# Kernel tuning notes

Hardware: AMD Instinct MI355X
Metric: run time of the kernel (lower is better)

The kernel has to match this reference:

```python
import jax, jax.numpy as jnp
import numpy as np
import math

B, S, D, H = 2, 2048, 512, 8
DH = D // H  # 64

def setup_inputs() -> dict:
    key = jax.random.key(0)
    ks = jax.random.split(key, 7)
    x = jax.random.normal(ks[0], (B, S, D), jnp.float32)
    shift = jax.random.normal(ks[1], (B, S, S), jnp.float32)
    mask = jax.random.randint(ks[2], (B, S, S), 0, 2).astype(jnp.float32)
    W = jax.random.normal(ks[3], (3 * D, D), jnp.float32) / math.sqrt(D)
    b = jnp.zeros((3 * D,), jnp.float32)
    Wo = jax.random.normal(ks[4], (D, D), jnp.float32) / math.sqrt(D)
    bo = jnp.zeros((D,), jnp.float32)
    return {"x": x, "shift": shift, "mask": mask, "W": W, "b": b, "Wo": Wo, "bo": bo}

def reference(x, shift, mask, W, b, Wo, bo):
    # qkv projection: (B,S,3D). torch chunk(n_heads) then chunk(3) =>
    # per-head layout is [q_h | k_h | v_h] within each 3*DH-sized slice.
    qkv = x @ W.T + b
    qkv = qkv.reshape(B, S, H, 3, DH)
    qkv = jnp.moveaxis(qkv, (2, 3), (0, 1))  # (H, 3, B, S, DH)
    q, k, v = qkv[:, 0], qkv[:, 1], qkv[:, 2]  # each (H, B, S, DH)

    head_scale = jnp.exp2(-jnp.arange(H, dtype=jnp.float32)).reshape(H, 1, 1, 1)  # 2^-h
    logits = jnp.einsum('hbqd,hbkd->hbqk', q, k) / math.sqrt(DH)
    logits = logits - head_scale * shift[None]          # ALiBi-style per-head shift
    m = mask[None]                                       # (1,B,S,S)
    logits = logits * m - 1e8 * (1.0 - m)
    att = jax.nn.softmax(logits, axis=-1)
    o = jnp.einsum('hbqk,hbkd->hbqd', att, v)            # (H,B,S,DH)
    o = jnp.moveaxis(o, 0, 2).reshape(B, S, D)           # concat heads on last dim
    return o @ Wo.T + bo
```

## Files before the change

kernel.cpp:

```cpp
#include <hip/hip_runtime.h>
#include <math.h>

constexpr int Bc = 2, Sc = 2048, Dc = 512, Hc = 8, DHc = 64;
constexpr int NQKV = 3 * Dc;

typedef unsigned short u16;
typedef unsigned int u32;
typedef __attribute__((ext_vector_type(8))) __bf16 bf16x8;
typedef __attribute__((ext_vector_type(16))) float f32x16;

#define MFMA32 __builtin_amdgcn_mfma_f32_32x32x16_bf16

__device__ inline uint2 splitpack2(float a, float b) {
  u32 ua = __float_as_uint(a), ub = __float_as_uint(b);
  u32 hi = (ub & 0xFFFF0000u) | (ua >> 16);
  float ra = a - __uint_as_float(ua & 0xFFFF0000u);
  float rb = b - __uint_as_float(ub & 0xFFFF0000u);
  u32 lo = (__float_as_uint(rb) & 0xFFFF0000u) | (__float_as_uint(ra) >> 16);
  return uint2{hi, lo};
}
__device__ inline void split1(float v, u16& hi, u16& lo) {
  u32 u = __float_as_uint(v);
  hi = (u16)(u >> 16);
  float r = v - __uint_as_float(u & 0xFFFF0000u);
  lo = (u16)(__float_as_uint(r) >> 16);
}

__global__ __launch_bounds__(256, 2) void gemm1_mfma(
    const float* __restrict__ x, const float* __restrict__ W,
    const float* __restrict__ bias, u16* __restrict__ Qhi,
    u16* __restrict__ Qlo, u16* __restrict__ Khi, u16* __restrict__ Klo,
    u16* __restrict__ Vthi, u16* __restrict__ Vtlo) {
  __shared__ __align__(16) u16 pool[18432];
  const int tid = threadIdx.x;
  const int wave = tid >> 6, lane = tid & 63, l31 = lane & 31, lhi = lane >> 5;
  const int wm = wave >> 1, wn = wave & 1;
  const int m0 = blockIdx.y * 128, n0 = blockIdx.x * 64;

  f32x16 acc[2];
#pragma unroll
  for (int r = 0; r < 16; ++r) {
    acc[0][r] = 0.f;
    acc[1][r] = 0.f;
  }

  for (int k0 = 0; k0 < 512; k0 += 32) {
#pragma unroll
    for (int i = 0; i < 2; ++i) {
      const int g = i * 256 + tid;
      const int m = g >> 2, kg = g & 3;
      const float* src = x + (size_t)(m0 + m) * 512 + k0 + kg * 8;
      const float4 v0 = *(const float4*)src;
      const float4 v1 = *(const float4*)(src + 4);
      const uint2 p0 = splitpack2(v0.x, v0.y), p1 = splitpack2(v0.z, v0.w);
      const uint2 p2 = splitpack2(v1.x, v1.y), p3 = splitpack2(v1.z, v1.w);
      const int row = (kg & 1) * 32 + (m & 31);
      *(uint4*)&pool[((((0 * 4 + (m >> 5)) * 2 + (kg >> 1)) * 64 + row)) * 8] =
          uint4{p0.x, p1.x, p2.x, p3.x};
      *(uint4*)&pool[((((1 * 4 + (m >> 5)) * 2 + (kg >> 1)) * 64 + row)) * 8] =
          uint4{p0.y, p1.y, p2.y, p3.y};
    }
    {
      const int n = tid >> 2, kg = tid & 3;
      const float* src = W + (size_t)(n0 + n) * 512 + k0 + kg * 8;
      const float4 v0 = *(const float4*)src;
      const float4 v1 = *(const float4*)(src + 4);
      const uint2 p0 = splitpack2(v0.x, v0.y), p1 = splitpack2(v0.z, v0.w);
      const uint2 p2 = splitpack2(v1.x, v1.y), p3 = splitpack2(v1.z, v1.w);
      const int row = (kg & 1) * 32 + (n & 31);
      *(uint4*)&pool[8192 +
                     ((((0 * 2 + (n >> 5)) * 2 + (kg >> 1)) * 64 + row)) * 8] =
          uint4{p0.x, p1.x, p2.x, p3.x};
      *(uint4*)&pool[8192 +
                     ((((1 * 2 + (n >> 5)) * 2 + (kg >> 1)) * 64 + row)) * 8] =
          uint4{p0.y, p1.y, p2.y, p3.y};
    }
    __syncthreads();
#pragma unroll
    for (int t = 0; t < 2; ++t) {
      const bf16x8 bh =
          *(const bf16x8*)&pool[8192 + (((0 * 2 + wn) * 2 + t) * 64 + lane) * 8];
      const bf16x8 bl =
          *(const bf16x8*)&pool[8192 + (((1 * 2 + wn) * 2 + t) * 64 + lane) * 8];
#pragma unroll
      for (int ti = 0; ti < 2; ++ti) {
        const bf16x8 ah =
            *(const bf16x8*)&pool[(((0 * 4 + wm * 2 + ti) * 2 + t) * 64 + lane) * 8];
        const bf16x8 al =
            *(const bf16x8*)&pool[(((1 * 4 + wm * 2 + ti) * 2 + t) * 64 + lane) * 8];
        acc[ti] = MFMA32(ah, bh, acc[ti], 0, 0, 0);
        acc[ti] = MFMA32(ah, bl, acc[ti], 0, 0, 0);
        acc[ti] = MFMA32(al, bh, acc[ti], 0, 0, 0);
      }
    }
    __syncthreads();
  }

  const int n = n0 + wn * 32 + l31;
  const float bn = bias[n];
  const int h = n0 / 192;
  const int t3 = (n0 % 192) / 64;
  const int dh = wn * 32 + l31;
  const int batch = m0 >> 11;
  const int s0 = m0 & 2047;
  const int hbq = h * 2 + batch;

#pragma unroll
  for (int ti = 0; ti < 2; ++ti)
#pragma unroll
    for (int r = 0; r < 16; ++r) {
      const int tl = wm * 64 + ti * 32 + (r & 3) + 8 * (r >> 2) + 4 * lhi;
      float val = acc[ti][r] + bn;
      if (t3 == 0) val *= 0.125f;
      u16 hi, lo;
      split1(val, hi, lo);
      pool[tl * 72 + dh] = hi;
      pool[9216 + tl * 72 + dh] = lo;
    }
  __syncthreads();

  u16 *d0, *d1;
  if (t3 == 0) {
    d0 = Qhi;
    d1 = Qlo;
  } else if (t3 == 1) {
    d0 = Khi;
    d1 = Klo;
  } else {
    d0 = Vthi;
    d1 = Vtlo;
  }

  if (t3 != 2) {
    const size_t base = ((size_t)hbq * 2048 + s0) * 64;
#pragma unroll
    for (int p = 0; p < 2; ++p) {
      u16* dst = (p ? d1 : d0) + base;
#pragma unroll
      for (int j = 0; j < 4; ++j) {
        const int g = tid * 32 + j * 8;
        const int token = g >> 6, dh8 = g & 63;
        *(uint4*)(dst + g) = *(const uint4*)&pool[p * 9216 + token * 72 + dh8];
      }
    }
  } else {
    const int d = tid >> 2, tp = (tid & 3) * 32;
#pragma unroll
    for (int p = 0; p < 2; ++p) {
      u16* dst = (p ? d1 : d0) + ((size_t)hbq * 64 + d) * 2048 + s0 + tp;
      u32 w[16];
#pragma unroll
      for (int j = 0; j < 16; ++j) {
        const u16 a = pool[p * 9216 + (tp + 2 * j) * 72 + d];
        const u16 b2 = pool[p * 9216 + (tp + 2 * j + 1) * 72 + d];
        w[j] = (u32)a | ((u32)b2 << 16);
      }
#pragma unroll
      for (int j = 0; j < 4; ++j)
        *(uint4*)(dst + j * 8) =
            uint4{w[4 * j], w[4 * j + 1], w[4 * j + 2], w[4 * j + 3]};
    }
  }
}

constexpr int KF0 = 8320;
constexpr int VF0 = 16512;
constexpr int PF0 = 24704;

#define ISSUE_TILE(KT)                                   \
  {                                                      \
    const float* sp_ = shr + (KT);                       \
    const float* mp_ = mkr + (KT);                       \
    pS0 = *(const float4*)(sp_);                         \
    pS1 = *(const float4*)(sp_ + 4);                     \
    pS2 = *(const float4*)(sp_ + 8);                     \
    pS3 = *(const float4*)(sp_ + 12);                    \
    pM0 = *(const float4*)(mp_);                         \
    pM1 = *(const float4*)(mp_ + 4);                     \
    pM2 = *(const float4*)(mp_ + 8);                     \
    pM3 = *(const float4*)(mp_ + 12);                    \
    const u16* h_ = kvsrc_hi + (size_t)(KT) * ktmul;     \
    const u16* l_ = kvsrc_lo + (size_t)(KT) * ktmul;     \
    pK0 = *(const uint4*)(h_);                           \
    pK1 = *(const uint4*)(l_);                           \
    pK2 = *(const uint4*)(h_ + 8);                       \
    pK3 = *(const uint4*)(l_ + 8);                       \
    pK4 = *(const uint4*)(h_ + 16);                      \
    pK5 = *(const uint4*)(l_ + 16);                      \
    pK6 = *(const uint4*)(h_ + 24);                      \
    pK7 = *(const uint4*)(l_ + 24);                      \
  }

#define COMMIT_TILE()                                    \
  {                                                      \
    smd[0 * 65] = (pM0.x != 0.f) ? pS0.x : 1e13f;        \
    smd[1 * 65] = (pM0.y != 0.f) ? pS0.y : 1e13f;        \
    smd[2 * 65] = (pM0.z != 0.f) ? pS0.z : 1e13f;        \
    smd[3 * 65] = (pM0.w != 0.f) ? pS0.w : 1e13f;        \
    smd[4 * 65] = (pM1.x != 0.f) ? pS1.x : 1e13f;        \
    smd[5 * 65] = (pM1.y != 0.f) ? pS1.y : 1e13f;        \
    smd[6 * 65] = (pM1.z != 0.f) ? pS1.z : 1e13f;        \
    smd[7 * 65] = (pM1.w != 0.f) ? pS1.w : 1e13f;        \
    smd[8 * 65] = (pM2.x != 0.f) ? pS2.x : 1e13f;        \
    smd[9 * 65] = (pM2.y != 0.f) ? pS2.y : 1e13f;        \
    smd[10 * 65] = (pM2.z != 0.f) ? pS2.z : 1e13f;       \
    smd[11 * 65] = (pM2.w != 0.f) ? pS2.w : 1e13f;       \
    smd[12 * 65] = (pM3.x != 0.f) ? pS3.x : 1e13f;       \
    smd[13 * 65] = (pM3.y != 0.f) ? pS3.y : 1e13f;       \
    smd[14 * 65] = (pM3.z != 0.f) ? pS3.z : 1e13f;       \
    smd[15 * 65] = (pM3.w != 0.f) ? pS3.w : 1e13f;       \
    *(uint4*)(kvdst + 0) = pK0;                          \
    *(uint4*)(kvdst + 4096) = pK1;                       \
    *(uint4*)(kvdst + 256) = pK2;                        \
    *(uint4*)(kvdst + 4096 + 256) = pK3;                 \
    *(uint4*)(kvdst + 512) = pK4;                        \
    *(uint4*)(kvdst + 4096 + 512) = pK5;                 \
    *(uint4*)(kvdst + 768) = pK6;                        \
    *(uint4*)(kvdst + 4096 + 768) = pK7;                 \
  }

__global__ __launch_bounds__(256, 2) void attn_mfma(
    const u16* __restrict__ Qhi, const u16* __restrict__ Qlo,
    const u16* __restrict__ Khi, const u16* __restrict__ Klo,
    const u16* __restrict__ Vthi, const u16* __restrict__ Vtlo,
    const float* __restrict__ shift, const float* __restrict__ mask,
    u16* __restrict__ Othi, u16* __restrict__ Otlo) {
  const int head = blockIdx.z, b = blockIdx.y, qb = blockIdx.x;
  const int tid = threadIdx.x;
  const int wave = tid >> 6;
  const int wq = wave >> 1, wk = wave & 1;
  const int lane = tid & 63;
  const int l31 = lane & 31, lhi = lane >> 5;

  __shared__ __align__(16) u16 smem[32896];
  float* SMs = (float*)smem;
  u16* Pw = smem + PF0 + wave * 2048;

  const size_t hb = (size_t)head * Bc + b;
  const int ql = wq * 32 + l31;
  const int qg = qb * 64 + ql;

  bf16x8 qf[2][4];
  {
    const size_t qbase = (hb * Sc + qg) * DHc;
#pragma unroll
    for (int t = 0; t < 4; ++t) {
      qf[0][t] = *(const bf16x8*)(Qhi + qbase + t * 16 + lhi * 8);
      qf[1][t] = *(const bf16x8*)(Qlo + qbase + t * 16 + lhi * 8);
    }
  }
  const float hs = exp2f(-(float)head);

  const int smq = tid >> 2, smk = (tid & 3) * 16;
  const float* shr = shift + ((size_t)b * Sc + qb * 64 + smq) * Sc + smk;
  const float* mkr = mask + ((size_t)b * Sc + qb * 64 + smq) * Sc + smk;
  float* const smd = SMs + (size_t)smk * 65 + smq;

  const int kr = lane >> 1, kh2 = lane & 1;
  const size_t kfix = (hb * Sc + wk * 32 + kr) * 64 + kh2 * 32;
  const size_t vfix = (hb * 64 + lane) * 2048 + wk * 32;
  const int vmt = lane >> 5, vdl = lane & 31;

  const u16* const kvsrc_hi = (wq == 0) ? (Khi + kfix) : (Vthi + vfix);
  const u16* const kvsrc_lo = (wq == 0) ? (Klo + kfix) : (Vtlo + vfix);
  const int ktmul = (wq == 0) ? 64 : 1;
  u16* const kvdst = (wq == 0)
                         ? &smem[KF0 + (wk * 4 + kh2 * 2) * 512 + kr * 8]
                         : &smem[VF0 + (wk * 4 + vmt * 2) * 512 + vdl * 8];

  float m_run = -INFINITY, l_run = 0.f;
  f32x16 o0, o1;
#pragma unroll
  for (int i = 0; i < 16; ++i) {
    o0[i] = 0.f;
    o1[i] = 0.f;
  }

  float4 pS0, pS1, pS2, pS3, pM0, pM1, pM2, pM3;
  uint4 pK0, pK1, pK2, pK3, pK4, pK5, pK6, pK7;

  ISSUE_TILE(0);
  for (int it = 0; it < 32; ++it) {
    COMMIT_TILE();
    __syncthreads();
    if (it < 31) ISSUE_TILE(it * 64 + 64);

    f32x16 s;
#pragma unroll
    for (int i = 0; i < 16; ++i) s[i] = 0.f;
#pragma unroll
    for (int t = 0; t < 4; ++t) {
      const bf16x8 kh = *(const bf16x8*)&smem[KF0 +
          (((0 * 2 + wk) * 4 + t) * 64 + lane) * 8];
      const bf16x8 kl = *(const bf16x8*)&smem[KF0 +
          (((1 * 2 + wk) * 4 + t) * 64 + lane) * 8];
      s = MFMA32(kh, qf[0][t], s, 0, 0, 0);
      s = MFMA32(kh, qf[1][t], s, 0, 0, 0);
      s = MFMA32(kl, qf[0][t], s, 0, 0, 0);
    }

    float p[16];
    float kmax = -INFINITY;
#pragma unroll
    for (int c = 0; c < 4; ++c) {
#pragma unroll
      for (int e = 0; e < 4; ++e) {
        const int kl_ = wk * 32 + c * 8 + lhi * 4 + e;
        const float a = hs * SMs[(size_t)kl_ * 65 + ql];
        const float lg = s[4 * c + e] - a;
        p[4 * c + e] = lg;
        kmax = fmaxf(kmax, lg);
      }
    }
    kmax = fmaxf(kmax, __shfl_xor(kmax, 32, 64));
    const float mnew = fmaxf(m_run, kmax);
    const float alpha = __expf(m_run - mnew);
    float rsum = 0.f;
#pragma unroll
    for (int r = 0; r < 16; ++r) {
      p[r] = __expf(p[r] - mnew);
      rsum += p[r];
    }
    rsum += __shfl_xor(rsum, 32, 64);
    l_run = l_run * alpha + rsum;
    m_run = mnew;
#pragma unroll
    for (int i = 0; i < 16; ++i) {
      o0[i] *= alpha;
      o1[i] *= alpha;
    }

#pragma unroll
    for (int c = 0; c < 4; ++c) {
      const uint2 s01 = splitpack2(p[4 * c + 0], p[4 * c + 1]);
      const uint2 s23 = splitpack2(p[4 * c + 2], p[4 * c + 3]);
      const int t = c >> 1, lh = c & 1;
      const int bi = (t * 64 + lh * 32 + l31) * 8 + lhi * 4;
      *(uint2*)&Pw[bi] = uint2{s01.x, s23.x};
      *(uint2*)&Pw[1024 + bi] = uint2{s01.y, s23.y};
    }

#pragma unroll
    for (int t = 0; t < 2; ++t) {
      const bf16x8 ph = *(const bf16x8*)&Pw[(t * 64 + lane) * 8];
      const bf16x8 pl_ = *(const bf16x8*)&Pw[1024 + (t * 64 + lane) * 8];
      bf16x8 vh = *(const bf16x8*)&smem[VF0 +
          ((((0 * 2 + wk) * 2 + 0) * 2 + t) * 64 + lane) * 8];
      bf16x8 vl = *(const bf16x8*)&smem[VF0 +
          ((((1 * 2 + wk) * 2 + 0) * 2 + t) * 64 + lane) * 8];
      o0 = MFMA32(vh, ph, o0, 0, 0, 0);
      o0 = MFMA32(vh, pl_, o0, 0, 0, 0);
      o0 = MFMA32(vl, ph, o0, 0, 0, 0);
      vh = *(const bf16x8*)&smem[VF0 +
          ((((0 * 2 + wk) * 2 + 1) * 2 + t) * 64 + lane) * 8];
      vl = *(const bf16x8*)&smem[VF0 +
          ((((1 * 2 + wk) * 2 + 1) * 2 + t) * 64 + lane) * 8];
      o1 = MFMA32(vh, ph, o1, 0, 0, 0);
      o1 = MFMA32(vh, pl_, o1, 0, 0, 0);
      o1 = MFMA32(vl, ph, o1, 0, 0, 0);
    }
    __syncthreads();
  }

  float* mL = (float*)(smem + KF0);
  float* lL = mL + 64;
  float* Om = lL + 64;
  if (wk == 1) {
    if (lhi == 0) {
      mL[wq * 32 + l31] = m_run;
      lL[wq * 32 + l31] = l_run;
    }
#pragma unroll
    for (int mt = 0; mt < 2; ++mt)
#pragma unroll
      for (int r = 0; r < 16; ++r) {
        const int row = mt * 32 + (r & 3) + 8 * (r >> 2) + 4 * lhi;
        Om[(wq * 64 + row) * 33 + l31] = (mt ? o1[r] : o0[r]);
      }
  }
  __syncthreads();
  if (wk == 0) {
    const float m1 = mL[wq * 32 + l31];
    const float l1v = lL[wq * 32 + l31];
    const float mst = fmaxf(m_run, m1);
    const float a0 = __expf(m_run - mst), a1 = __expf(m1 - mst);
    const float inv = 1.f / (a0 * l_run + a1 * l1v);
    const int tok = b * 2048 + qg;
#pragma unroll
    for (int mt = 0; mt < 2; ++mt)
#pragma unroll
      for (int r = 0; r < 16; ++r) {
        const int row = mt * 32 + (r & 3) + 8 * (r >> 2) + 4 * lhi;
        const float val = (a0 * (mt ? o1[r] : o0[r]) +
                           a1 * Om[(wq * 64 + row) * 33 + l31]) *
                          inv;
        const int d = head * 64 + row;
        u16 hi, lo;
        split1(val, hi, lo);
        const size_t idx = ((size_t)(d >> 3) * 4096 + tok) * 8 + (d & 7);
        Othi[idx] = hi;
        Otlo[idx] = lo;
      }
  }
}

__global__ __launch_bounds__(256, 2) void gemm2_mfma(
    const u16* __restrict__ Othi, const u16* __restrict__ Otlo,
    const float* __restrict__ Wo, const float* __restrict__ bo,
    float* __restrict__ out) {
  __shared__ __align__(16) u16 Af[2][2][2][64][8];
  __shared__ __align__(16) u16 Bf[2][2][2][64][8];
  const int tid = threadIdx.x;
  const int wave = tid >> 6, lane = tid & 63, l31 = lane & 31, lhi = lane >> 5;
  const int wm = wave >> 1, wn = wave & 1;
  const int m0 = blockIdx.y * 64, n0 = blockIdx.x * 64;

  f32x16 acc;
#pragma unroll
  for (int r = 0; r < 16; ++r) acc[r] = 0.f;

  for (int k0 = 0; k0 < 512; k0 += 32) {
#pragma unroll
    for (int i = 0; i < 2; ++i) {
      const int f = i * 256 + tid;
      const int p = f >> 8, rem = f & 255, c = rem >> 6, tok = rem & 63;
      const u16* src =
          (p ? Otlo : Othi) + ((size_t)(k0 / 8 + c) * 4096 + m0 + tok) * 8;
      *(uint4*)&Af[p][tok >> 5][c >> 1][(c & 1) * 32 + (tok & 31)][0] =
          *(const uint4*)src;
    }
    {
      const int n = tid >> 2, c = tid & 3;
      const float* src = Wo + (size_t)(n0 + n) * 512 + k0 + c * 8;
      const float4 v0 = *(const float4*)src;
      const float4 v1 = *(const float4*)(src + 4);
      const uint2 q0 = splitpack2(v0.x, v0.y), q1 = splitpack2(v0.z, v0.w);
      const uint2 q2 = splitpack2(v1.x, v1.y), q3 = splitpack2(v1.z, v1.w);
      *(uint4*)&Bf[0][n >> 5][c >> 1][(c & 1) * 32 + (n & 31)][0] =
          uint4{q0.x, q1.x, q2.x, q3.x};
      *(uint4*)&Bf[1][n >> 5][c >> 1][(c & 1) * 32 + (n & 31)][0] =
          uint4{q0.y, q1.y, q2.y, q3.y};
    }
    __syncthreads();
#pragma unroll
    for (int t = 0; t < 2; ++t) {
      const bf16x8 ah = *(const bf16x8*)&Af[0][wm][t][lane][0];
      const bf16x8 al = *(const bf16x8*)&Af[1][wm][t][lane][0];
      const bf16x8 bh = *(const bf16x8*)&Bf[0][wn][t][lane][0];
      const bf16x8 bl = *(const bf16x8*)&Bf[1][wn][t][lane][0];
      acc = MFMA32(ah, bh, acc, 0, 0, 0);
      acc = MFMA32(ah, bl, acc, 0, 0, 0);
      acc = MFMA32(al, bh, acc, 0, 0, 0);
    }
    __syncthreads();
  }

  const int n = n0 + wn * 32 + l31;
  const float bn = bo[n];
#pragma unroll
  for (int r = 0; r < 16; ++r) {
    const int m = m0 + wm * 32 + (r & 3) + 8 * (r >> 2) + 4 * lhi;
    out[(size_t)m * 512 + n] = acc[r] + bn;
  }
}

extern "C" void kernel_launch(void* const* d_in, const int* in_sizes, int n_in,
                              void* d_out, int out_size, void* d_ws,
                              size_t ws_size, hipStream_t stream) {
  const float* x = (const float*)d_in[0];
  const float* shift = (const float*)d_in[1];
  const float* mask = (const float*)d_in[2];
  const float* W = (const float*)d_in[3];
  const float* b = (const float*)d_in[4];
  const float* Wo = (const float*)d_in[5];
  const float* bo = (const float*)d_in[6];
  float* out = (float*)d_out;

  const size_t P = (size_t)Hc * Bc * Sc * DHc;
  u16* ws0 = (u16*)d_ws;
  u16* Qhi = ws0;
  u16* Qlo = ws0 + P;
  u16* Khi = ws0 + 2 * P;
  u16* Klo = ws0 + 3 * P;
  u16* Vthi = ws0 + 4 * P;
  u16* Vtlo = ws0 + 5 * P;
  u16* Othi = ws0 + 6 * P;
  u16* Otlo = ws0 + 7 * P;

  gemm1_mfma<<<dim3(NQKV / 64, (Bc * Sc) / 128), 256, 0, stream>>>(
      x, W, b, Qhi, Qlo, Khi, Klo, Vthi, Vtlo);

  attn_mfma<<<dim3(Sc / 64, Bc, Hc), 256, 0, stream>>>(
      Qhi, Qlo, Khi, Klo, Vthi, Vtlo, shift, mask, Othi, Otlo);

  gemm2_mfma<<<dim3(Dc / 64, (Bc * Sc) / 64), 256, 0, stream>>>(Othi, Otlo, Wo,
                                                                bo, out);
}
```

Baseline: 251.3 us.

## Presplit GEMM inputs, prefetch gemm1 tiles, and keep attention P in registers

Adds a presplit kernel that converts x and W to bf16 hi/lo pairs once, writing them to workspace and to the output buffer as scratch. gemm1 then loads the pre-split data with register prefetching of the next k-tile. In attention, the P matrix is rebuilt with cross-lane shuffles instead of being staged through LDS, which cuts shared memory enough to allow occupancy 3. The attention kernel also raises wave priority around the MFMA sections. These changes remove per-tile conversion work and LDS round trips, at the cost of an extra kernel launch and extra global traffic for the split copies.

```diff
diff --git a/kernel.cpp b/kernel.cpp
--- a/kernel.cpp
+++ b/kernel.cpp
@@ -26,8 +26,53 @@
   lo = (u16)(__float_as_uint(r) >> 16);
 }
 
-__global__ __launch_bounds__(256, 2) void gemm1_mfma(
+__global__ __launch_bounds__(256) void presplit_xw(
     const float* __restrict__ x, const float* __restrict__ W,
+    u16* __restrict__ Xhi, u16* __restrict__ Xlo, u16* __restrict__ Whi,
+    u16* __restrict__ Wlo) {
+  const u32 g = blockIdx.x * 256 + threadIdx.x;
+  const float* src;
+  u16 *dh, *dl;
+  if (g < 262144u) {
+    src = x + (size_t)g * 8;
+    dh = Xhi + (size_t)g * 8;
+    dl = Xlo + (size_t)g * 8;
+  } else {
+    const u32 gw = g - 262144u;
+    src = W + (size_t)gw * 8;
+    dh = Whi + (size_t)gw * 8;
+    dl = Wlo + (size_t)gw * 8;
+  }
+  const float4 v0 = *(const float4*)src;
+  const float4 v1 = *(const float4*)(src + 4);
+  const uint2 p0 = splitpack2(v0.x, v0.y), p1 = splitpack2(v0.z, v0.w);
+  const uint2 p2 = splitpack2(v1.x, v1.y), p3 = splitpack2(v1.z, v1.w);
+  *(uint4*)dh = uint4{p0.x, p1.x, p2.x, p3.x};
+  *(uint4*)dl = uint4{p0.y, p1.y, p2.y, p3.y};
+}
+
+#define G1_ISSUE(K0)                          \
+  {                                           \
+    a0h = *(const uint4*)(srcA0h + (K0));     \
+    a0l = *(const uint4*)(srcA0l + (K0));     \
+    a1h = *(const uint4*)(srcA1h + (K0));     \
+    a1l = *(const uint4*)(srcA1l + (K0));     \
+    b0h = *(const uint4*)(srcBh + (K0));      \
+    b0l = *(const uint4*)(srcBl + (K0));      \
+  }
+#define G1_COMMIT()                           \
+  {                                           \
+    *(uint4*)dA0h = a0h;                      \
+    *(uint4*)dA0l = a0l;                      \
+    *(uint4*)dA1h = a1h;                      \
+    *(uint4*)dA1l = a1l;                      \
+    *(uint4*)dBh = b0h;                       \
+    *(uint4*)dBl = b0l;                       \
+  }
+
+__global__ __launch_bounds__(256, 3) void gemm1_mfma(
+    const u16* __restrict__ Xhi, const u16* __restrict__ Xlo,
+    const u16* __restrict__ Whi, const u16* __restrict__ Wlo,
     const float* __restrict__ bias, u16* __restrict__ Qhi,
     u16* __restrict__ Qlo, u16* __restrict__ Khi, u16* __restrict__ Klo,
     u16* __restrict__ Vthi, u16* __restrict__ Vtlo) {
@@ -37,6 +82,22 @@
   const int wm = wave >> 1, wn = wave & 1;
   const int m0 = blockIdx.y * 128, n0 = blockIdx.x * 64;
 
+  const int mA = tid >> 2, kgA = tid & 3;
+  const int rowA = (kgA & 1) * 32 + (mA & 31);
+  u16* const dA0h = &pool[(((mA >> 5) * 2 + (kgA >> 1)) * 64 + rowA) * 8];
+  u16* const dA0l = dA0h + 4096;
+  u16* const dA1h =
+      &pool[(((2 + (mA >> 5)) * 2 + (kgA >> 1)) * 64 + rowA) * 8];
+  u16* const dA1l = dA1h + 4096;
+  u16* const dBh = &pool[8192 + (((mA >> 5) * 2 + (kgA >> 1)) * 64 + rowA) * 8];
+  u16* const dBl = dBh + 2048;
+  const u16* const srcA0h = Xhi + (size_t)(m0 + mA) * 512 + kgA * 8;
+  const u16* const srcA0l = Xlo + (size_t)(m0 + mA) * 512 + kgA * 8;
+  const u16* const srcA1h = srcA0h + 64 * 512;
+  const u16* const srcA1l = srcA0l + 64 * 512;
+  const u16* const srcBh = Whi + (size_t)(n0 + mA) * 512 + kgA * 8;
+  const u16* const srcBl = Wlo + (size_t)(n0 + mA) * 512 + kgA * 8;
+
   f32x16 acc[2];
 #pragma unroll
   for (int r = 0; r < 16; ++r) {
@@ -44,38 +105,12 @@
     acc[1][r] = 0.f;
   }
 
+  uint4 a0h, a0l, a1h, a1l, b0h, b0l;
+  G1_ISSUE(0);
   for (int k0 = 0; k0 < 512; k0 += 32) {
-#pragma unroll
-    for (int i = 0; i < 2; ++i) {
-      const int g = i * 256 + tid;
-      const int m = g >> 2, kg = g & 3;
-      const float* src = x + (size_t)(m0 + m) * 512 + k0 + kg * 8;
-      const float4 v0 = *(const float4*)src;
-      const float4 v1 = *(const float4*)(src + 4);
-      const uint2 p0 = splitpack2(v0.x, v0.y), p1 = splitpack2(v0.z, v0.w);
-      const uint2 p2 = splitpack2(v1.x, v1.y), p3 = splitpack2(v1.z, v1.w);
-      const int row = (kg & 1) * 32 + (m & 31);
-      *(uint4*)&pool[((((0 * 4 + (m >> 5)) * 2 + (kg >> 1)) * 64 + row)) * 8] =
-          uint4{p0.x, p1.x, p2.x, p3.x};
-      *(uint4*)&pool[((((1 * 4 + (m >> 5)) * 2 + (kg >> 1)) * 64 + row)) * 8] =
-          uint4{p0.y, p1.y, p2.y, p3.y};
-    }
-    {
-      const int n = tid >> 2, kg = tid & 3;
-      const float* src = W + (size_t)(n0 + n) * 512 + k0 + kg * 8;
-      const float4 v0 = *(const float4*)src;
-      const float4 v1 = *(const float4*)(src + 4);
-      const uint2 p0 = splitpack2(v0.x, v0.y), p1 = splitpack2(v0.z, v0.w);
-      const uint2 p2 = splitpack2(v1.x, v1.y), p3 = splitpack2(v1.z, v1.w);
-      const int row = (kg & 1) * 32 + (n & 31);
-      *(uint4*)&pool[8192 +
-                     ((((0 * 2 + (n >> 5)) * 2 + (kg >> 1)) * 64 + row)) * 8] =
-          uint4{p0.x, p1.x, p2.x, p3.x};
-      *(uint4*)&pool[8192 +
-                     ((((1 * 2 + (n >> 5)) * 2 + (kg >> 1)) * 64 + row)) * 8] =
-          uint4{p0.y, p1.y, p2.y, p3.y};
-    }
+    G1_COMMIT();
     __syncthreads();
+    if (k0 < 480) G1_ISSUE(k0 + 32);
 #pragma unroll
     for (int t = 0; t < 2; ++t) {
       const bf16x8 bh =
@@ -165,7 +200,6 @@
 
 constexpr int KF0 = 8320;
 constexpr int VF0 = 16512;
-constexpr int PF0 = 24704;
 
 #define ISSUE_TILE(KT)                                   \
   {                                                      \
@@ -219,7 +253,15 @@
     *(uint4*)(kvdst + 4096 + 768) = pK7;                 \
   }
 
-__global__ __launch_bounds__(256, 2) void attn_mfma(
+__device__ inline void xchg32(u32 own0, u32 own1, bool hiHalf, u32& wA,
+                              u32& wB) {
+  const u32 q0 = (u32)__shfl_xor((int)own0, 32, 64);
+  const u32 q1 = (u32)__shfl_xor((int)own1, 32, 64);
+  wA = hiHalf ? q1 : own0;
+  wB = hiHalf ? own1 : q0;
+}
+
+__global__ __launch_bounds__(256, 3) void attn_mfma(
     const u16* __restrict__ Qhi, const u16* __restrict__ Qlo,
     const u16* __restrict__ Khi, const u16* __restrict__ Klo,
     const u16* __restrict__ Vthi, const u16* __restrict__ Vtlo,
@@ -232,9 +274,8 @@
   const int lane = tid & 63;
   const int l31 = lane & 31, lhi = lane >> 5;
 
-  __shared__ __align__(16) u16 smem[32896];
+  __shared__ __align__(16) u16 smem[24704];
   float* SMs = (float*)smem;
-  u16* Pw = smem + PF0 + wave * 2048;
 
   const size_t hb = (size_t)head * Bc + b;
   const int ql = wq * 32 + l31;
@@ -279,6 +320,8 @@
   float4 pS0, pS1, pS2, pS3, pM0, pM1, pM2, pM3;
   uint4 pK0, pK1, pK2, pK3, pK4, pK5, pK6, pK7;
 
+  const bool hiHalf = (lhi != 0);
+
   ISSUE_TILE(0);
   for (int it = 0; it < 32; ++it) {
     COMMIT_TILE();
@@ -288,6 +331,7 @@
     f32x16 s;
 #pragma unroll
     for (int i = 0; i < 16; ++i) s[i] = 0.f;
+    __builtin_amdgcn_s_setprio(1);
 #pragma unroll
     for (int t = 0; t < 4; ++t) {
       const bf16x8 kh = *(const bf16x8*)&smem[KF0 +
@@ -298,6 +342,7 @@
       s = MFMA32(kh, qf[1][t], s, 0, 0, 0);
       s = MFMA32(kl, qf[0][t], s, 0, 0, 0);
     }
+    __builtin_amdgcn_s_setprio(0);
 
     float p[16];
     float kmax = -INFINITY;
@@ -330,20 +375,23 @@
       o1[i] *= alpha;
     }
 
-#pragma unroll
-    for (int c = 0; c < 4; ++c) {
-      const uint2 s01 = splitpack2(p[4 * c + 0], p[4 * c + 1]);
-      const uint2 s23 = splitpack2(p[4 * c + 2], p[4 * c + 3]);
-      const int t = c >> 1, lh = c & 1;
-      const int bi = (t * 64 + lh * 32 + l31) * 8 + lhi * 4;
-      *(uint2*)&Pw[bi] = uint2{s01.x, s23.x};
-      *(uint2*)&Pw[1024 + bi] = uint2{s01.y, s23.y};
-    }
-
+    __builtin_amdgcn_s_setprio(1);
 #pragma unroll
     for (int t = 0; t < 2; ++t) {
-      const bf16x8 ph = *(const bf16x8*)&Pw[(t * 64 + lane) * 8];
-      const bf16x8 pl_ = *(const bf16x8*)&Pw[1024 + (t * 64 + lane) * 8];
+      const uint2 Av = splitpack2(p[8 * t + 0], p[8 * t + 1]);
+      const uint2 Bv = splitpack2(p[8 * t + 2], p[8 * t + 3]);
+      const uint2 Cv = splitpack2(p[8 * t + 4], p[8 * t + 5]);
+      const uint2 Dv = splitpack2(p[8 * t + 6], p[8 * t + 7]);
+      u32 w0h, w1h, w2h, w3h, w0l, w1l, w2l, w3l;
+      xchg32(Av.x, Cv.x, hiHalf, w0h, w2h);
+      xchg32(Bv.x, Dv.x, hiHalf, w1h, w3h);
+      xchg32(Av.y, Cv.y, hiHalf, w0l, w2l);
+      xchg32(Bv.y, Dv.y, hiHalf, w1l, w3l);
+      const uint4 phw = uint4{w0h, w1h, w2h, w3h};
+      const uint4 plw = uint4{w0l, w1l, w2l, w3l};
+      const bf16x8 ph = *(const bf16x8*)&phw;
+      const bf16x8 pl_ = *(const bf16x8*)&plw;
+
       bf16x8 vh = *(const bf16x8*)&smem[VF0 +
           ((((0 * 2 + wk) * 2 + 0) * 2 + t) * 64 + lane) * 8];
       bf16x8 vl = *(const bf16x8*)&smem[VF0 +
@@ -359,6 +407,7 @@
       o1 = MFMA32(vh, pl_, o1, 0, 0, 0);
       o1 = MFMA32(vl, ph, o1, 0, 0, 0);
     }
+    __builtin_amdgcn_s_setprio(0);
     __syncthreads();
   }
 
@@ -486,9 +535,15 @@
   u16* Vtlo = ws0 + 5 * P;
   u16* Othi = ws0 + 6 * P;
   u16* Otlo = ws0 + 7 * P;
+  u16* Xhi = ws0 + 6 * P;
+  u16* Xlo = ws0 + 7 * P;
+  u16* Whi = (u16*)out;
+  u16* Wlo = (u16*)out + 786432;
+
+  presplit_xw<<<dim3(1408), 256, 0, stream>>>(x, W, Xhi, Xlo, Whi, Wlo);
 
   gemm1_mfma<<<dim3(NQKV / 64, (Bc * Sc) / 128), 256, 0, stream>>>(
-      x, W, b, Qhi, Qlo, Khi, Klo, Vthi, Vtlo);
+      Xhi, Xlo, Whi, Wlo, b, Qhi, Qlo, Khi, Klo, Vthi, Vtlo);
 
   attn_mfma<<<dim3(Sc / 64, Bc, Hc), 256, 0, stream>>>(
       Qhi, Qlo, Khi, Klo, Vthi, Vtlo, shift, mask, Othi, Otlo);
```

Result: slower. 319.9 us (+27.3%).
